# Performance work log

Hardware: AMD Instinct MI355X
Metric: run time of the kernel (lower is better)

The kernel has to match this reference:

```python
import jax, jax.numpy as jnp
import numpy as np

B, S, D, E, N, R = 2, 1024, 1024, 2048, 16, 64
EPS = 1e-5


def setup_inputs() -> dict:
    key = jax.random.key(0)
    ks = jax.random.split(key, 16)
    f = lambda k, sh, s=0.02: (jax.random.normal(k, sh, jnp.float32) * s)
    Alog = jnp.log(jnp.tile(jnp.arange(1, N + 1, dtype=jnp.float32), (E, 1)))  # [E,N]
    return dict(
        x=f(ks[0], (B, S, D), 1.0),
        c=f(ks[1], (B, 2 * D), 1.0),
        w=f(ks[2], (B, D), 1.0),
        norm1_g=jnp.ones((D,)), norm1_b=jnp.zeros((D,)),
        norm2_g=jnp.ones((D,)), norm2_b=jnp.zeros((D,)),
        Wx=f(ks[3], (E, D)), bx=jnp.zeros((E,)),
        Wz=f(ks[4], (E, D)), bz=jnp.zeros((E,)),
        Wf=f(ks[5], (D, E)), bf=jnp.zeros((D,)),
        Wada=f(ks[6], (3 * D, 2 * D)), bada=jnp.zeros((3 * D,)),
        Wc1=f(ks[7], (E, E)), bc1=jnp.zeros((E,)),
        Wc2=f(ks[8], (E, E)), bc2=jnp.zeros((E,)),
        Wdbc1=f(ks[9], (R + 2 * N, E)), Wdt1=f(ks[10], (E, R)), bdt1=jnp.zeros((E,)),
        Alog1=Alog, Dp1=jnp.ones((E,)),
        Wdbc2=f(ks[11], (R + 2 * N, E)), Wdt2=f(ks[12], (E, R)), bdt2=jnp.zeros((E,)),
        Alog2=Alog, Dp2=jnp.ones((E,)),
    )


def _ln(x, g, b):
    m = jnp.mean(x, -1, keepdims=True)
    v = jnp.mean((x - m) ** 2, -1, keepdims=True)
    return (x - m) * jax.lax.rsqrt(v + EPS) * g + b


def _ssm(u, Wdbc, Wdt, bdt, Alog, Dp):
    # u: [b,s,e] -> selective scan (mamba-minimal math)
    dbc = jnp.einsum('bse,re->bsr', u, Wdbc)                      # [b,s,R+2N]
    dlt, Bm, Cm = jnp.split(dbc, [R, R + N], axis=-1)
    delta = jax.nn.softplus(jnp.einsum('bsr,er->bse', dlt, Wdt) + bdt)  # [b,s,e]
    A = -jnp.exp(Alog)                                            # [e,n]
    dA = jnp.exp(delta[..., None] * A)                            # [b,s,e,n]
    dBu = delta[..., None] * Bm[:, :, None, :] * u[..., None]     # [b,s,e,n]

    def step(h, xs):
        dA_t, dBu_t, C_t = xs
        h = dA_t * h + dBu_t                                      # [b,e,n]
        y = jnp.einsum('ben,bn->be', h, C_t)
        return h, y

    h0 = jnp.zeros((u.shape[0], u.shape[2], N), u.dtype)
    _, ys = jax.lax.scan(step, h0, (dA.swapaxes(0, 1), dBu.swapaxes(0, 1), Cm.swapaxes(0, 1)))
    return ys.swapaxes(0, 1) + u * Dp


def reference(x, c, w, norm1_g, norm1_b, norm2_g, norm2_b, Wx, bx, Wz, bz, Wf, bf,
              Wada, bada, Wc1, bc1, Wc2, bc2,
              Wdbc1, Wdt1, bdt1, Alog1, Dp1, Wdbc2, Wdt2, bdt2, Alog2, Dp2):
    ada = jax.nn.silu(c) @ Wada.T + bada                          # [b,3D]
    shift, scale, gate = jnp.split(ada, 3, axis=1)
    x_ssm = _ln(x, norm1_g, norm1_b)
    x_ssm = x_ssm * (1.0 + scale[:, None, :]) + shift[:, None, :]
    skip = x_ssm
    x_ssm = _ln(x_ssm, norm2_g, norm2_b)
    mz = jnp.einsum('bsd,ed->bse', x_ssm, Wz) + bz                # proj_z
    mx = jnp.einsum('bsd,ed->bse', x_ssm, Wx) + bx                # proj_x
    act_mx = jax.nn.silu(mx)
    # forward branch: conv1d(k=1) is per-position linear over channels
    z1 = jnp.einsum('bse,fe->bsf', mz, Wc1) + bc1
    z1 = _ssm(z1, Wdbc1, Wdt1, bdt1, Alog1, Dp1)
    y1 = act_mx * z1
    # backward branch
    z2 = jnp.einsum('bse,fe->bsf', mz, Wc2) + bc2
    z2 = jnp.flip(z2, axis=1)
    z2 = _ssm(z2, Wdbc2, Wdt2, bdt2, Alog2, Dp2)
    z2 = jnp.flip(z2, axis=1)
    y2 = act_mx * z2
    out = jnp.einsum('bse,de->bsd', y1 + y2, Wf) + bf + skip
    return x + gate[:, None, :] * out
```

## Files before the change

### kernel.cpp

```cpp
#include <hip/hip_runtime.h>
#include <hip/hip_bf16.h>

#define EPSQ 1e-5f
#define B_ 2
#define S_ 1024
#define D_ 1024
#define E_ 2048
#define N_ 16
#define R_ 64
#define M_ 2048
#define CS_ 64
#define NC_ 16
#define CH_ 4096
#define KSPLIT_ 8
#define KCH_ 256
#define KS3_ 4
#define KC3_ 512

typedef float f32x4 __attribute__((ext_vector_type(4)));
typedef short s16x8 __attribute__((ext_vector_type(8)));
typedef unsigned short u16;

#define GLDS(g, l)                                                              \
  __builtin_amdgcn_global_load_lds(                                             \
      (const __attribute__((address_space(1))) void*)(g),                       \
      (__attribute__((address_space(3))) void*)(l), 16, 0, 0)

static __device__ __forceinline__ short f2bf_s(float f) {
  __hip_bfloat16 h = __float2bfloat16(f);
  return *reinterpret_cast<short*>(&h);
}

static __device__ __forceinline__ s16x8 cvt8(float4 a, float4 b) {
  s16x8 r;
  r[0] = f2bf_s(a.x); r[1] = f2bf_s(a.y); r[2] = f2bf_s(a.z); r[3] = f2bf_s(a.w);
  r[4] = f2bf_s(b.x); r[5] = f2bf_s(b.y); r[6] = f2bf_s(b.z); r[7] = f2bf_s(b.w);
  return r;
}

static __device__ __forceinline__ float block_sum(float v, float* red) {
  int t = threadIdx.x;
  red[t] = v;
  __syncthreads();
  #pragma unroll
  for (int off = 128; off > 0; off >>= 1) {
    if (t < off) red[t] += red[t + off];
    __syncthreads();
  }
  float r = red[0];
  __syncthreads();
  return r;
}

__global__ void k_wcvt_all(const float* __restrict__ Wz, const float* __restrict__ Wx,
                           const float* __restrict__ Wc1, const float* __restrict__ Wc2,
                           const float* __restrict__ Wf, u16* __restrict__ Wzxb,
                           u16* __restrict__ Wcb, u16* __restrict__ Wfb) {
  int i = blockIdx.x * 256 + threadIdx.x;
  const float* src; u16* dst; int off;
  if (i < 262144)        { src = Wz;  dst = Wzxb;           off = i; }
  else if (i < 524288)   { src = Wx;  dst = Wzxb + 2097152; off = i - 262144; }
  else if (i < 1048576)  { src = Wc1; dst = Wcb;            off = i - 524288; }
  else if (i < 1572864)  { src = Wc2; dst = Wcb + 4194304;  off = i - 1048576; }
  else                   { src = Wf;  dst = Wfb;            off = i - 1572864; }
  float4 a = ((const float4*)src)[2 * off];
  float4 b = ((const float4*)src)[2 * off + 1];
  ((s16x8*)dst)[off] = cvt8(a, b);
}

__global__ void k_ada(const float* __restrict__ c, const float* __restrict__ Wada,
                      const float* __restrict__ bada, float* __restrict__ ada) {
  __shared__ float red[256];
  int j = blockIdx.x;
  const float* wrow = Wada + (size_t)j * (2 * D_);
  float acc0 = 0.f, acc1 = 0.f;
  for (int i = threadIdx.x; i < 2 * D_; i += 256) {
    float w = wrow[i];
    float c0 = c[i];
    float c1 = c[2 * D_ + i];
    acc0 += (c0 / (1.f + __expf(-c0))) * w;
    acc1 += (c1 / (1.f + __expf(-c1))) * w;
  }
  float t0 = block_sum(acc0, red);
  float t1 = block_sum(acc1, red);
  if (threadIdx.x == 0) {
    float bv = bada[j];
    ada[j] = t0 + bv;
    ada[(size_t)(3 * D_) + j] = t1 + bv;
  }
}

__global__ void k_ln(const float* __restrict__ x,
                     const float* __restrict__ g1, const float* __restrict__ b1,
                     const float* __restrict__ g2, const float* __restrict__ b2,
                     const float* __restrict__ ada,
                     float* __restrict__ skip, u16* __restrict__ xs2b) {
  __shared__ float red[256];
  int row = blockIdx.x;
  int b = row >> 10;
  int t = threadIdx.x;
  const float* xr = x + (size_t)row * D_;

  float v[4];
  float4 xv = *(const float4*)(xr + t * 4);
  v[0] = xv.x; v[1] = xv.y; v[2] = xv.z; v[3] = xv.w;

  float s = v[0] + v[1] + v[2] + v[3];
  float mean = block_sum(s, red) * (1.f / D_);
  float q = 0.f;
  #pragma unroll
  for (int i = 0; i < 4; ++i) { float d = v[i] - mean; q += d * d; }
  float var = block_sum(q, red) * (1.f / D_);
  float rstd = rsqrtf(var + EPSQ);

  const float* shf = ada + (size_t)b * (3 * D_);
  const float* scl = shf + D_;
  float s2 = 0.f;
  #pragma unroll
  for (int i = 0; i < 4; ++i) {
    int d = t * 4 + i;
    float xn = (v[i] - mean) * rstd * g1[d] + b1[d];
    float tt = xn * (1.f + scl[d]) + shf[d];
    v[i] = tt;
    s2 += tt;
    skip[(size_t)row * D_ + d] = tt;
  }
  float mean2 = block_sum(s2, red) * (1.f / D_);
  float q2 = 0.f;
  #pragma unroll
  for (int i = 0; i < 4; ++i) { float d = v[i] - mean2; q2 += d * d; }
  float var2 = block_sum(q2, red) * (1.f / D_);
  float rstd2 = rsqrtf(var2 + EPSQ);
  short4 o;
  float o0 = (v[0] - mean2) * rstd2 * g2[t * 4 + 0] + b2[t * 4 + 0];
  float o1 = (v[1] - mean2) * rstd2 * g2[t * 4 + 1] + b2[t * 4 + 1];
  float o2 = (v[2] - mean2) * rstd2 * g2[t * 4 + 2] + b2[t * 4 + 2];
  float o3 = (v[3] - mean2) * rstd2 * g2[t * 4 + 3] + b2[t * 4 + 3];
  o.x = f2bf_s(o0); o.y = f2bf_s(o1); o.z = f2bf_s(o2); o.w = f2bf_s(o3);
  *(short4*)((short*)xs2b + (size_t)row * D_ + t * 4) = o;
}

template <int MODE>
__global__ __launch_bounds__(256, 2) void k_mgemm(
    const u16* __restrict__ A, int lda,
    const u16* __restrict__ W,
    const float* __restrict__ b0, const float* __restrict__ b1,
    void* __restrict__ C0p, float* __restrict__ C1, int Nh, int K,
    int nbx, int nby) {
  __shared__ __align__(16) u16 lA[2][4096];
  __shared__ __align__(16) u16 lB[2][4096];
  const int t = threadIdx.x;
  const int lane = t & 63, wid = t >> 6;
  const int wr = wid >> 1, wc = wid & 1;

  int nwg = gridDim.x;
  int hw = blockIdx.x;
  int swz = (hw & 7) * (nwg >> 3) + (hw >> 3);
  int by = swz % nby;
  int rst = swz / nby;
  int bx = rst % nbx;
  int bz = rst / nbx;
  const int m0 = by * 128, n0 = bx * 128;
  const int kb = (MODE == 2) ? bz * KC3_ : 0;
  const int KT = (MODE == 2) ? (KC3_ / 32) : (K / 32);

  f32x4 acc[4][4];
  #pragma unroll
  for (int m = 0; m < 4; ++m)
    #pragma unroll
    for (int n = 0; n < 4; ++n) acc[m][n] = (f32x4){0.f, 0.f, 0.f, 0.f};

  const int frow = lane & 15, fkg = lane >> 4;
  int aoff[4], boff[4];
  #pragma unroll
  for (int m = 0; m < 4; ++m) {
    int row = wr * 64 + m * 16 + frow;
    aoff[m] = (row * 64 + fkg * 16) ^ ((row & 7) << 4);
  }
  #pragma unroll
  for (int n = 0; n < 4; ++n) {
    int col = wc * 64 + n * 16 + frow;
    boff[n] = (col * 64 + fkg * 16) ^ ((col & 7) << 4);
  }

  const int d = lane;
  const int rl = (((d >> 2) ^ (d >> 4)) & 1) | (((d >> 3) & 1) << 1) |
                 (((d >> 4) & 1) << 2) | (((d >> 5) & 1) << 3);
  const int cc = ((d ^ (d >> 2) ^ (d >> 4)) & 1) |
                 ((((d >> 1) ^ (d >> 3)) & 1) << 1);
  const u16* gA0 = A + (size_t)(m0 + wid * 16 + rl) * lda + kb + cc * 8;
  const u16* gA1 = A + (size_t)(m0 + (wid + 4) * 16 + rl) * lda + kb + cc * 8;
  const u16* gB0 = W + (size_t)(n0 + wid * 16 + rl) * K + kb + cc * 8;
  const u16* gB1 = W + (size_t)(n0 + (wid + 4) * 16 + rl) * K + kb + cc * 8;

  #define STAGE_(buf, kk)                                   \
    do {                                                    \
      GLDS(gA0 + (kk), &lA[buf][wid * 512]);                \
      GLDS(gA1 + (kk), &lA[buf][(wid + 4) * 512]);          \
      GLDS(gB0 + (kk), &lB[buf][wid * 512]);                \
      GLDS(gB1 + (kk), &lB[buf][(wid + 4) * 512]);          \
    } while (0)

  STAGE_(0, 0);
  __syncthreads();

  for (int kt = 0; kt < KT; ++kt) {
    const int cur = kt & 1, nxt = cur ^ 1;
    if (kt + 1 < KT) {
      if (nxt) STAGE_(1, (kt + 1) * 32);
      else     STAGE_(0, (kt + 1) * 32);
    }
    s16x8 af[4], bfr[4];
    #pragma unroll
    for (int m = 0; m < 4; ++m) af[m] = *(const s16x8*)((const char*)lA[cur] + aoff[m]);
    #pragma unroll
    for (int n = 0; n < 4; ++n) bfr[n] = *(const s16x8*)((const char*)lB[cur] + boff[n]);
    #pragma unroll
    for (int m = 0; m < 4; ++m)
      #pragma unroll
      for (int n = 0; n < 4; ++n)
        acc[m][n] = __builtin_amdgcn_mfma_f32_16x16x32_bf16(af[m], bfr[n], acc[m][n], 0, 0, 0);
    __syncthreads();
  }
  #undef STAGE_

  #pragma unroll
  for (int m = 0; m < 4; ++m) {
    int rbase = m0 + wr * 64 + m * 16 + fkg * 4;
    #pragma unroll
    for (int n = 0; n < 4; ++n) {
      int colG = n0 + wc * 64 + n * 16 + frow;
      bool second = (MODE != 2) && (colG >= Nh);
      int colL = second ? colG - Nh : colG;
      float bv = (MODE != 2) ? (second ? b1[colL] : b0[colL]) : 0.f;
      #pragma unroll
      for (int j = 0; j < 4; ++j) {
        int row = rbase + j;
        float v = acc[m][n][j] + bv;
        if constexpr (MODE == 2) {
          ((float*)C0p)[(size_t)bz * ((size_t)M_ * Nh) + (size_t)row * Nh + colG] = v;
        } else if constexpr (MODE == 1) {
          if (second) {
            v = v / (1.f + __expf(-v));
            C1[(size_t)row * Nh + colL] = v;
          } else {
            ((u16*)C0p)[(size_t)row * Nh + colL] = (u16)f2bf_s(v);
          }
        } else {
          if (second) C1[(size_t)row * Nh + colL] = v;
          else ((float*)C0p)[(size_t)row * Nh + colL] = v;
        }
      }
    }
  }
}

__global__ void k_out_red(const float* __restrict__ Part, const float* __restrict__ bfb,
                          const float* __restrict__ skip, const float* __restrict__ x,
                          const float* __restrict__ ada, float* __restrict__ out) {
  int i = blockIdx.x * 256 + threadIdx.x;
  const int PL = M_ * D_ / 4;
  int c4 = i & (D_ / 4 - 1);
  int row = i >> 8;
  int b = row >> 10;
  const f32x4* P = (const f32x4*)Part;
  f32x4 v = P[i];
  #pragma unroll
  for (int kz = 1; kz < KS3_; ++kz) v += P[(size_t)kz * PL + i];
  f32x4 bv = ((const f32x4*)bfb)[c4];
  f32x4 sv = ((const f32x4*)skip)[i];
  f32x4 xv = ((const f32x4*)x)[i];
  f32x4 gv = ((const f32x4*)(ada + (size_t)b * (3 * D_) + 2 * D_))[c4];
  f32x4 o = v + bv + sv;
  ((f32x4*)out)[i] = xv + gv * o;
}

__global__ void k_dbc_split(const float* __restrict__ z1, const float* __restrict__ z2,
                            const float* __restrict__ W1, const float* __restrict__ W2,
                            float* __restrict__ Part) {
  const int BK = 16;
  __shared__ float As[BK][65];
  __shared__ float Bs[BK][65];
  int n0 = blockIdx.x * 64, m0 = blockIdx.y * 64;
  int br = blockIdx.z >> 3;
  int kbase = (blockIdx.z & 7) * KCH_;
  const float* A = br ? z2 : z1;
  const float* W = br ? W2 : W1;
  int t = threadIdx.x;
  int tx = t & 15, ty = t >> 4;
  int ar = t >> 2, ac4 = (t & 3) * 4;
  float acc[4][4] = {};

  for (int k0 = 0; k0 < KCH_; k0 += BK) {
    const float* ap = A + (size_t)(m0 + ar) * E_ + kbase + k0 + ac4;
    float4 av = *(const float4*)ap;
    As[ac4 + 0][ar] = av.x; As[ac4 + 1][ar] = av.y;
    As[ac4 + 2][ar] = av.z; As[ac4 + 3][ar] = av.w;

    int wn = n0 + ar;
    if (wn < 96) {
      const float* wp = W + (size_t)wn * E_ + kbase + k0 + ac4;
      float4 wv = *(const float4*)wp;
      Bs[ac4 + 0][ar] = wv.x; Bs[ac4 + 1][ar] = wv.y;
      Bs[ac4 + 2][ar] = wv.z; Bs[ac4 + 3][ar] = wv.w;
    } else {
      Bs[ac4 + 0][ar] = 0.f; Bs[ac4 + 1][ar] = 0.f;
      Bs[ac4 + 2][ar] = 0.f; Bs[ac4 + 3][ar] = 0.f;
    }
    __syncthreads();
    #pragma unroll
    for (int kk = 0; kk < BK; ++kk) {
      float a0 = As[kk][ty * 4 + 0], a1 = As[kk][ty * 4 + 1];
      float a2 = As[kk][ty * 4 + 2], a3 = As[kk][ty * 4 + 3];
      float c0 = Bs[kk][tx * 4 + 0], c1 = Bs[kk][tx * 4 + 1];
      float c2 = Bs[kk][tx * 4 + 2], c3 = Bs[kk][tx * 4 + 3];
      acc[0][0] += a0 * c0; acc[0][1] += a0 * c1; acc[0][2] += a0 * c2; acc[0][3] += a0 * c3;
      acc[1][0] += a1 * c0; acc[1][1] += a1 * c1; acc[1][2] += a1 * c2; acc[1][3] += a1 * c3;
      acc[2][0] += a2 * c0; acc[2][1] += a2 * c1; acc[2][2] += a2 * c2; acc[2][3] += a2 * c3;
      acc[3][0] += a3 * c0; acc[3][1] += a3 * c1; acc[3][2] += a3 * c2; acc[3][3] += a3 * c3;
    }
    __syncthreads();
  }

  #pragma unroll
  for (int i = 0; i < 4; ++i) {
    int row = m0 + ty * 4 + i;
    #pragma unroll
    for (int j = 0; j < 4; ++j) {
      int col = n0 + tx * 4 + j;
      if (col < 96)
        Part[(size_t)blockIdx.z * (M_ * 96) + (size_t)row * 96 + col] = acc[i][j];
    }
  }
}

__global__ void k_dbc_reduce(const float* __restrict__ Part, float* __restrict__ dbc1,
                             float* __restrict__ dbc2) {
  int idx = blockIdx.x * 256 + threadIdx.x;
  const int tot = M_ * 96;
  int br = idx >= tot;
  int i = br ? idx - tot : idx;
  const float* base = Part + (size_t)(br ? 8 : 0) * tot;
  float s = 0.f;
  #pragma unroll
  for (int kz = 0; kz < KSPLIT_; ++kz) s += base[(size_t)kz * tot + i];
  (br ? dbc2 : dbc1)[i] = s;
}

__global__ void k_dlt(const float* __restrict__ dbc1, const float* __restrict__ dbc2,
                      const float* __restrict__ Wdt1, const float* __restrict__ Wdt2,
                      const float* __restrict__ bdt1, const float* __restrict__ bdt2,
                      float* __restrict__ dlt1, float* __restrict__ dlt2) {
  const int BK = 16;
  __shared__ float As[BK][65];
  __shared__ float Bs[BK][65];
  int br = blockIdx.z;
  const float* A = br ? dbc2 : dbc1;
  const float* W = br ? Wdt2 : Wdt1;
  const float* bias = br ? bdt2 : bdt1;
  float* C = br ? dlt2 : dlt1;
  int n0 = blockIdx.x * 64, m0 = blockIdx.y * 64;
  int t = threadIdx.x;
  int tx = t & 15, ty = t >> 4;
  int ar = t >> 2, ac4 = (t & 3) * 4;
  float acc[4][4] = {};

  for (int k0 = 0; k0 < R_; k0 += BK) {
    const float* ap = A + (size_t)(m0 + ar) * 96 + k0 + ac4;
    float4 av = *(const float4*)ap;
    As[ac4 + 0][ar] = av.x; As[ac4 + 1][ar] = av.y;
    As[ac4 + 2][ar] = av.z; As[ac4 + 3][ar] = av.w;

    const float* wp = W + (size_t)(n0 + ar) * R_ + k0 + ac4;
    float4 wv = *(const float4*)wp;
    Bs[ac4 + 0][ar] = wv.x; Bs[ac4 + 1][ar] = wv.y;
    Bs[ac4 + 2][ar] = wv.z; Bs[ac4 + 3][ar] = wv.w;
    __syncthreads();
    #pragma unroll
    for (int kk = 0; kk < BK; ++kk) {
      float a0 = As[kk][ty * 4 + 0], a1 = As[kk][ty * 4 + 1];
      float a2 = As[kk][ty * 4 + 2], a3 = As[kk][ty * 4 + 3];
      float c0 = Bs[kk][tx * 4 + 0], c1 = Bs[kk][tx * 4 + 1];
      float c2 = Bs[kk][tx * 4 + 2], c3 = Bs[kk][tx * 4 + 3];
      acc[0][0] += a0 * c0; acc[0][1] += a0 * c1; acc[0][2] += a0 * c2; acc[0][3] += a0 * c3;
      acc[1][0] += a1 * c0; acc[1][1] += a1 * c1; acc[1][2] += a1 * c2; acc[1][3] += a1 * c3;
      acc[2][0] += a2 * c0; acc[2][1] += a2 * c1; acc[2][2] += a2 * c2; acc[2][3] += a2 * c3;
      acc[3][0] += a3 * c0; acc[3][1] += a3 * c1; acc[3][2] += a3 * c2; acc[3][3] += a3 * c3;
    }
    __syncthreads();
  }

  #pragma unroll
  for (int i = 0; i < 4; ++i) {
    int row = m0 + ty * 4 + i;
    #pragma unroll
    for (int j = 0; j < 4; ++j) {
      int col = n0 + tx * 4 + j;
      float v = acc[i][j] + bias[col];
      v = (v > 20.f) ? v : log1pf(__expf(v));
      C[(size_t)row * E_ + col] = v;
    }
  }
}

__global__ void k_scan_chunk(const float* __restrict__ z1, const float* __restrict__ z2,
                             const float* __restrict__ dlt1, const float* __restrict__ dlt2,
                             const float* __restrict__ dbc1, const float* __restrict__ dbc2,
                             const float* __restrict__ Alog1, const float* __restrict__ Alog2,
                             float* __restrict__ Pb1, float* __restrict__ Pb2,
                             float* __restrict__ Hb1, float* __restrict__ Hb2) {
  int br = blockIdx.x >> 10;
  int bidx = blockIdx.x & 1023;
  const float* u    = br ? z2 : z1;
  const float* dlt  = br ? dlt2 : dlt1;
  const float* dbc  = br ? dbc2 : dbc1;
  const float* Alog = br ? Alog2 : Alog1;
  float* Pbuf = br ? Pb2 : Pb1;
  float* Hbuf = br ? Hb2 : Hb1;
  int tid = threadIdx.x;
  int q = tid & 3, chl = tid >> 2;
  int ch = (bidx & 63) * 64 + chl;
  int c  = bidx >> 6;
  int b = ch >> 11, e = ch & (E_ - 1);
  int nb = q * 4;
  float A[4], P[4], h[4];
  #pragma unroll
  for (int i = 0; i < 4; ++i) {
    A[i] = -__expf(Alog[(size_t)e * N_ + nb + i]);
    P[i] = 1.f; h[i] = 0.f;
  }
  for (int t = 0; t < CS_; ++t) {
    int tau = c * CS_ + t;
    int s = br ? (S_ - 1 - tau) : tau;
    size_t row = (size_t)b * S_ + s;
    float uu = u[row * E_ + e];
    float delta = dlt[row * E_ + e];
    float du = delta * uu;
    float4 Bm = *(const float4*)(dbc + row * 96 + 64 + nb);
    const float bmv[4] = {Bm.x, Bm.y, Bm.z, Bm.w};
    #pragma unroll
    for (int i = 0; i < 4; ++i) {
      float dA = __expf(delta * A[i]);
      P[i] *= dA;
      h[i] = dA * h[i] + du * bmv[i];
    }
  }
  #pragma unroll
  for (int i = 0; i < 4; ++i) {
    size_t off = (size_t)(c * N_ + nb + i) * CH_ + ch;
    Pbuf[off] = P[i];
    Hbuf[off] = h[i];
  }
}

__global__ void k_scan_comb(float* __restrict__ Pb1, float* __restrict__ Pb2,
                            const float* __restrict__ Hb1, const float* __restrict__ Hb2) {
  int idx = blockIdx.x * 256 + threadIdx.x;
  int br = idx >> 16;
  int id = idx & 65535;
  float* Pbuf = br ? Pb2 : Pb1;
  const float* Hbuf = br ? Hb2 : Hb1;
  int ch = id & (CH_ - 1);
  int n  = id >> 12;
  float hcur = 0.f;
  for (int c = 0; c < NC_; ++c) {
    size_t off = (size_t)(c * N_ + n) * CH_ + ch;
    float p  = Pbuf[off];
    float hl = Hbuf[off];
    Pbuf[off] = hcur;
    hcur = p * hcur + hl;
  }
}

__global__ void k_scan_apply(float* __restrict__ z1, float* __restrict__ z2,
                             const float* __restrict__ dlt1, const float* __restrict__ dlt2,
                             const float* __restrict__ dbc1, const float* __restrict__ dbc2,
                             const float* __restrict__ Alog1, const float* __restrict__ Alog2,
                             const float* __restrict__ Dp1, const float* __restrict__ Dp2,
                             const float* __restrict__ Pb1, const float* __restrict__ Pb2) {
  int br = blockIdx.x >> 10;
  int bidx = blockIdx.x & 1023;
  float* u          = br ? z2 : z1;
  const float* dlt  = br ? dlt2 : dlt1;
  const float* dbc  = br ? dbc2 : dbc1;
  const float* Alog = br ? Alog2 : Alog1;
  const float* Dp   = br ? Dp2 : Dp1;
  const float* Pbuf = br ? Pb2 : Pb1;
  int tid = threadIdx.x;
  int q = tid & 3, chl = tid >> 2;
  int ch = (bidx & 63) * 64 + chl;
  int c  = bidx >> 6;
  int b = ch >> 11, e = ch & (E_ - 1);
  int nb = q * 4;
  float A[4], h[4];
  #pragma unroll
  for (int i = 0; i < 4; ++i) {
    A[i] = -__expf(Alog[(size_t)e * N_ + nb + i]);
    h[i] = Pbuf[(size_t)(c * N_ + nb + i) * CH_ + ch];
  }
  float dp = Dp[e];
  for (int t = 0; t < CS_; ++t) {
    int tau = c * CS_ + t;
    int s = br ? (S_ - 1 - tau) : tau;
    size_t row = (size_t)b * S_ + s;
    float uu = u[row * E_ + e];
    float delta = dlt[row * E_ + e];
    float du = delta * uu;
    float4 Bm = *(const float4*)(dbc + row * 96 + 64 + nb);
    float4 Cm = *(const float4*)(dbc + row * 96 + 80 + nb);
    const float bmv[4] = {Bm.x, Bm.y, Bm.z, Bm.w};
    const float cmv[4] = {Cm.x, Cm.y, Cm.z, Cm.w};
    float y = 0.f;
    #pragma unroll
    for (int i = 0; i < 4; ++i) {
      float dA = __expf(delta * A[i]);
      h[i] = dA * h[i] + du * bmv[i];
      y += h[i] * cmv[i];
    }
    y += __shfl_xor(y, 1);
    y += __shfl_xor(y, 2);
    if (q == 0) u[row * E_ + e] = y + uu * dp;
  }
}

__global__ void k_ysum(const float* __restrict__ z1, const float* __restrict__ z2,
                       const float* __restrict__ amx, u16* __restrict__ ybf) {
  int i = blockIdx.x * 256 + threadIdx.x;
  f32x4 a = ((const f32x4*)amx)[i];
  f32x4 p = ((const f32x4*)z1)[i] + ((const f32x4*)z2)[i];
  f32x4 v = a * p;
  short4 o;
  o.x = f2bf_s(v[0]); o.y = f2bf_s(v[1]); o.z = f2bf_s(v[2]); o.w = f2bf_s(v[3]);
  ((short4*)ybf)[i] = o;
}

extern "C" void kernel_launch(void* const* d_in, const int* in_sizes, int n_in,
                              void* d_out, int out_size, void* d_ws, size_t ws_size,
                              hipStream_t stream) {
  const float* x     = (const float*)d_in[0];
  const float* c     = (const float*)d_in[1];
  const float* n1g   = (const float*)d_in[3];
  const float* n1b   = (const float*)d_in[4];
  const float* n2g   = (const float*)d_in[5];
  const float* n2b   = (const float*)d_in[6];
  const float* Wx    = (const float*)d_in[7];
  const float* bx    = (const float*)d_in[8];
  const float* Wz    = (const float*)d_in[9];
  const float* bz    = (const float*)d_in[10];
  const float* Wf    = (const float*)d_in[11];
  const float* bfb   = (const float*)d_in[12];
  const float* Wada  = (const float*)d_in[13];
  const float* bada  = (const float*)d_in[14];
  const float* Wc1   = (const float*)d_in[15];
  const float* bc1   = (const float*)d_in[16];
  const float* Wc2   = (const float*)d_in[17];
  const float* bc2   = (const float*)d_in[18];
  const float* Wdbc1 = (const float*)d_in[19];
  const float* Wdt1  = (const float*)d_in[20];
  const float* bdt1  = (const float*)d_in[21];
  const float* Alog1 = (const float*)d_in[22];
  const float* Dp1   = (const float*)d_in[23];
  const float* Wdbc2 = (const float*)d_in[24];
  const float* Wdt2  = (const float*)d_in[25];
  const float* bdt2  = (const float*)d_in[26];
  const float* Alog2 = (const float*)d_in[27];
  const float* Dp2   = (const float*)d_in[28];

  const int M = M_;
  float* ws    = (float*)d_ws;
  float* ada   = ws;
  float* skip  = ada + 8192;
  float* xs2s  = skip + 2097152;
  float* mzs   = xs2s + 2097152;
  float* amx   = mzs + 4194304;
  float* z1    = amx + 4194304;
  float* z2    = z1 + 4194304;
  u16*   Wzxb  = (u16*)(z2 + 4194304);
  u16*   Wcb   = Wzxb + 4194304;
  u16*   Wfb   = Wcb + 8388608;

  u16*   xs2b  = (u16*)xs2s;
  u16*   mzb   = (u16*)mzs;
  float* dbc1  = xs2s;
  float* dbc2  = xs2s + 196608;
  float* Part  = mzs;
  float* dlt1  = mzs;
  float* dlt2  = (float*)Wcb;
  float* Part3 = mzs;
  float* Pb1   = (float*)d_out;
  float* Hb1   = (float*)d_out + 1048576;
  float* Pb2   = (float*)Wzxb;
  float* Hb2   = (float*)Wzxb + 1048576;
  u16*   ybf   = (u16*)d_out;

  k_wcvt_all<<<dim3(7168), 256, 0, stream>>>(Wz, Wx, Wc1, Wc2, Wf, Wzxb, Wcb, Wfb);
  k_ada<<<dim3(3 * D_), dim3(256), 0, stream>>>(c, Wada, bada, ada);
  k_ln<<<dim3(M), dim3(256), 0, stream>>>(x, n1g, n1b, n2g, n2b, ada, skip, xs2b);
  k_mgemm<1><<<dim3(512), 256, 0, stream>>>(xs2b, D_, Wzxb, bz, bx,
                                            (void*)mzb, amx, E_, D_, 32, 16);
  k_mgemm<0><<<dim3(512), 256, 0, stream>>>(mzb, E_, Wcb, bc1, bc2,
                                            (void*)z1, z2, E_, E_, 32, 16);
  k_dbc_split<<<dim3(2, M / 64, 16), 256, 0, stream>>>(z1, z2, Wdbc1, Wdbc2, Part);
  k_dbc_reduce<<<dim3(2 * M * 96 / 256), 256, 0, stream>>>(Part, dbc1, dbc2);
  k_dlt<<<dim3(E_ / 64, M / 64, 2), 256, 0, stream>>>(dbc1, dbc2, Wdt1, Wdt2,
                                                      bdt1, bdt2, dlt1, dlt2);
  k_scan_chunk<<<dim3(2048), dim3(256), 0, stream>>>(z1, z2, dlt1, dlt2, dbc1, dbc2,
                                                     Alog1, Alog2, Pb1, Pb2, Hb1, Hb2);
  k_scan_comb<<<dim3(512), dim3(256), 0, stream>>>(Pb1, Pb2, Hb1, Hb2);
  k_scan_apply<<<dim3(2048), dim3(256), 0, stream>>>(z1, z2, dlt1, dlt2, dbc1, dbc2,
                                                     Alog1, Alog2, Dp1, Dp2, Pb1, Pb2);
  k_ysum<<<dim3((M * E_) / 4 / 256), 256, 0, stream>>>(z1, z2, amx, ybf);
  k_mgemm<2><<<dim3(512), 256, 0, stream>>>(ybf, E_, Wfb, nullptr, nullptr,
                                            (void*)Part3, nullptr, D_, E_, 8, 16);
  k_out_red<<<dim3(M * D_ / 4 / 256), 256, 0, stream>>>(Part3, bfb, skip, x, ada,
                                                        (float*)d_out);
}
```

Measured before the change: 335.9 us.

## Replace scalar FP32 dbc projection GEMM with bf16 MFMA split-K kernel

Replaces the scalar FP32 split-K GEMM that computes the dbc projection (z times Wdbc, 96 output columns) with a kernel using bf16 16x16x32 MFMA instructions. Operands are converted from fp32 to bf16 on the fly into XOR-swizzled, double-buffered LDS tiles, with global loads prefetched two steps ahead. Tiles grow to 128 rows by 128 columns, so 32 of the 128 columns are zero padding and wasted work. The projection loses precision from bf16 inputs, and that error feeds delta and the scan.

```diff
diff --git a/kernel.cpp b/kernel.cpp
--- a/kernel.cpp
+++ b/kernel.cpp
@@ -255,6 +255,110 @@
   }
 }
 
+__global__ __launch_bounds__(256, 2) void k_dbc_mfma(
+    const float* __restrict__ z1, const float* __restrict__ z2,
+    const float* __restrict__ W1, const float* __restrict__ W2,
+    float* __restrict__ Part) {
+  __shared__ __align__(16) u16 lA[2][4096];
+  __shared__ __align__(16) u16 lB[2][4096];
+  const int t = threadIdx.x;
+  const int lane = t & 63, wid = t >> 6;
+  const int wr = wid >> 1, wc = wid & 1;
+  const int m0 = blockIdx.x * 128;
+  const int kb = blockIdx.y * KCH_;
+  const int br = blockIdx.z;
+  const float* A = br ? z2 : z1;
+  const float* W = br ? W2 : W1;
+  const int KT = KCH_ / 32;
+
+  f32x4 acc[4][4];
+  #pragma unroll
+  for (int m = 0; m < 4; ++m)
+    #pragma unroll
+    for (int n = 0; n < 4; ++n) acc[m][n] = (f32x4){0.f, 0.f, 0.f, 0.f};
+
+  const int frow = lane & 15, fkg = lane >> 4;
+  int aoff[4], boff[4];
+  #pragma unroll
+  for (int m = 0; m < 4; ++m) {
+    int row = wr * 64 + m * 16 + frow;
+    aoff[m] = (row * 64 + fkg * 16) ^ ((row & 7) << 4);
+  }
+  #pragma unroll
+  for (int n = 0; n < 4; ++n) {
+    int col = wc * 64 + n * 16 + frow;
+    boff[n] = (col * 64 + fkg * 16) ^ ((col & 7) << 4);
+  }
+
+  const int sr = t >> 2, sk = (t & 3) * 8;
+  const int w0 = (sr * 64 + (t & 3) * 16) ^ ((sr & 7) << 4);
+  const int w1o = w0 + 4096;
+  const bool v1 = (sr + 64) < 96;
+  const float* pa0 = A + (size_t)(m0 + sr) * E_ + kb + sk;
+  const float* pa1 = pa0 + (size_t)64 * E_;
+  const float* pb0 = W + (size_t)sr * E_ + kb + sk;
+  const float* pb1 = W + (size_t)(sr + 64) * E_ + kb + sk;
+  const float4 zf4 = {0.f, 0.f, 0.f, 0.f};
+
+  float4 a00 = *(const float4*)(pa0);     float4 a01 = *(const float4*)(pa0 + 4);
+  float4 a10 = *(const float4*)(pa1);     float4 a11 = *(const float4*)(pa1 + 4);
+  float4 b00 = *(const float4*)(pb0);     float4 b01 = *(const float4*)(pb0 + 4);
+  float4 b10 = v1 ? *(const float4*)(pb1) : zf4;
+  float4 b11 = v1 ? *(const float4*)(pb1 + 4) : zf4;
+  *(s16x8*)((char*)lA[0] + w0)  = cvt8(a00, a01);
+  *(s16x8*)((char*)lA[0] + w1o) = cvt8(a10, a11);
+  *(s16x8*)((char*)lB[0] + w0)  = cvt8(b00, b01);
+  *(s16x8*)((char*)lB[0] + w1o) = cvt8(b10, b11);
+  a00 = *(const float4*)(pa0 + 32);  a01 = *(const float4*)(pa0 + 36);
+  a10 = *(const float4*)(pa1 + 32);  a11 = *(const float4*)(pa1 + 36);
+  b00 = *(const float4*)(pb0 + 32);  b01 = *(const float4*)(pb0 + 36);
+  b10 = v1 ? *(const float4*)(pb1 + 32) : zf4;
+  b11 = v1 ? *(const float4*)(pb1 + 36) : zf4;
+
+  for (int kt = 0; kt < KT; ++kt) {
+    __syncthreads();
+    const int cur = kt & 1, nxt = cur ^ 1;
+    s16x8 af[4], bfr[4];
+    #pragma unroll
+    for (int m = 0; m < 4; ++m) af[m] = *(const s16x8*)((const char*)lA[cur] + aoff[m]);
+    #pragma unroll
+    for (int n = 0; n < 4; ++n) bfr[n] = *(const s16x8*)((const char*)lB[cur] + boff[n]);
+    if (kt + 1 < KT) {
+      *(s16x8*)((char*)lA[nxt] + w0)  = cvt8(a00, a01);
+      *(s16x8*)((char*)lA[nxt] + w1o) = cvt8(a10, a11);
+      *(s16x8*)((char*)lB[nxt] + w0)  = cvt8(b00, b01);
+      *(s16x8*)((char*)lB[nxt] + w1o) = cvt8(b10, b11);
+    }
+    if (kt + 2 < KT) {
+      int kn = (kt + 2) * 32;
+      a00 = *(const float4*)(pa0 + kn);  a01 = *(const float4*)(pa0 + kn + 4);
+      a10 = *(const float4*)(pa1 + kn);  a11 = *(const float4*)(pa1 + kn + 4);
+      b00 = *(const float4*)(pb0 + kn);  b01 = *(const float4*)(pb0 + kn + 4);
+      b10 = v1 ? *(const float4*)(pb1 + kn) : zf4;
+      b11 = v1 ? *(const float4*)(pb1 + kn + 4) : zf4;
+    }
+    #pragma unroll
+    for (int m = 0; m < 4; ++m)
+      #pragma unroll
+      for (int n = 0; n < 4; ++n)
+        acc[m][n] = __builtin_amdgcn_mfma_f32_16x16x32_bf16(af[m], bfr[n], acc[m][n], 0, 0, 0);
+  }
+
+  float* P = Part + (size_t)(br * 8 + blockIdx.y) * (M_ * 96);
+  #pragma unroll
+  for (int m = 0; m < 4; ++m) {
+    int rbase = m0 + wr * 64 + m * 16 + fkg * 4;
+    #pragma unroll
+    for (int n = 0; n < 4; ++n) {
+      int col = wc * 64 + n * 16 + frow;
+      if (col >= 96) continue;
+      #pragma unroll
+      for (int j = 0; j < 4; ++j)
+        P[(size_t)(rbase + j) * 96 + col] = acc[m][n][j];
+    }
+  }
+}
+
 __global__ void k_out_red(const float* __restrict__ Part, const float* __restrict__ bfb,
                           const float* __restrict__ skip, const float* __restrict__ x,
                           const float* __restrict__ ada, float* __restrict__ out) {
@@ -273,65 +377,6 @@
   f32x4 gv = ((const f32x4*)(ada + (size_t)b * (3 * D_) + 2 * D_))[c4];
   f32x4 o = v + bv + sv;
   ((f32x4*)out)[i] = xv + gv * o;
-}
-
-__global__ void k_dbc_split(const float* __restrict__ z1, const float* __restrict__ z2,
-                            const float* __restrict__ W1, const float* __restrict__ W2,
-                            float* __restrict__ Part) {
-  const int BK = 16;
-  __shared__ float As[BK][65];
-  __shared__ float Bs[BK][65];
-  int n0 = blockIdx.x * 64, m0 = blockIdx.y * 64;
-  int br = blockIdx.z >> 3;
-  int kbase = (blockIdx.z & 7) * KCH_;
-  const float* A = br ? z2 : z1;
-  const float* W = br ? W2 : W1;
-  int t = threadIdx.x;
-  int tx = t & 15, ty = t >> 4;
-  int ar = t >> 2, ac4 = (t & 3) * 4;
-  float acc[4][4] = {};
-
-  for (int k0 = 0; k0 < KCH_; k0 += BK) {
-    const float* ap = A + (size_t)(m0 + ar) * E_ + kbase + k0 + ac4;
-    float4 av = *(const float4*)ap;
-    As[ac4 + 0][ar] = av.x; As[ac4 + 1][ar] = av.y;
-    As[ac4 + 2][ar] = av.z; As[ac4 + 3][ar] = av.w;
-
-    int wn = n0 + ar;
-    if (wn < 96) {
-      const float* wp = W + (size_t)wn * E_ + kbase + k0 + ac4;
-      float4 wv = *(const float4*)wp;
-      Bs[ac4 + 0][ar] = wv.x; Bs[ac4 + 1][ar] = wv.y;
-      Bs[ac4 + 2][ar] = wv.z; Bs[ac4 + 3][ar] = wv.w;
-    } else {
-      Bs[ac4 + 0][ar] = 0.f; Bs[ac4 + 1][ar] = 0.f;
-      Bs[ac4 + 2][ar] = 0.f; Bs[ac4 + 3][ar] = 0.f;
-    }
-    __syncthreads();
-    #pragma unroll
-    for (int kk = 0; kk < BK; ++kk) {
-      float a0 = As[kk][ty * 4 + 0], a1 = As[kk][ty * 4 + 1];
-      float a2 = As[kk][ty * 4 + 2], a3 = As[kk][ty * 4 + 3];
-      float c0 = Bs[kk][tx * 4 + 0], c1 = Bs[kk][tx * 4 + 1];
-      float c2 = Bs[kk][tx * 4 + 2], c3 = Bs[kk][tx * 4 + 3];
-      acc[0][0] += a0 * c0; acc[0][1] += a0 * c1; acc[0][2] += a0 * c2; acc[0][3] += a0 * c3;
-      acc[1][0] += a1 * c0; acc[1][1] += a1 * c1; acc[1][2] += a1 * c2; acc[1][3] += a1 * c3;
-      acc[2][0] += a2 * c0; acc[2][1] += a2 * c1; acc[2][2] += a2 * c2; acc[2][3] += a2 * c3;
-      acc[3][0] += a3 * c0; acc[3][1] += a3 * c1; acc[3][2] += a3 * c2; acc[3][3] += a3 * c3;
-    }
-    __syncthreads();
-  }
-
-  #pragma unroll
-  for (int i = 0; i < 4; ++i) {
-    int row = m0 + ty * 4 + i;
-    #pragma unroll
-    for (int j = 0; j < 4; ++j) {
-      int col = n0 + tx * 4 + j;
-      if (col < 96)
-        Part[(size_t)blockIdx.z * (M_ * 96) + (size_t)row * 96 + col] = acc[i][j];
-    }
-  }
 }
 
 __global__ void k_dbc_reduce(const float* __restrict__ Part, float* __restrict__ dbc1,
@@ -600,7 +645,7 @@
                                             (void*)mzb, amx, E_, D_, 32, 16);
   k_mgemm<0><<<dim3(512), 256, 0, stream>>>(mzb, E_, Wcb, bc1, bc2,
                                             (void*)z1, z2, E_, E_, 32, 16);
-  k_dbc_split<<<dim3(2, M / 64, 16), 256, 0, stream>>>(z1, z2, Wdbc1, Wdbc2, Part);
+  k_dbc_mfma<<<dim3(16, 8, 2), 256, 0, stream>>>(z1, z2, Wdbc1, Wdbc2, Part);
   k_dbc_reduce<<<dim3(2 * M * 96 / 256), 256, 0, stream>>>(Part, dbc1, dbc2);
   k_dlt<<<dim3(E_ / 64, M / 64, 2), 256, 0, stream>>>(dbc1, dbc2, Wdt1, Wdt2,
                                                       bdt1, bdt2, dlt1, dlt2);
```

Measured after the change: 300.7 us. 1.12x faster.
